# Kernel optimization log

Hardware: AMD Instinct MI355X
Metric: run time of the kernel (lower is better)

Reference implementation:

```python
import jax, jax.numpy as jnp
import numpy as np

N = 100000
E = 1600000
IN_DIM = 128
HID = 64
NUM_CLASSES = 40
K = 3


def setup_inputs() -> dict:
    key = jax.random.key(0)
    ks = jax.random.split(key, 8)
    x = jax.random.normal(ks[0], (N, IN_DIM), dtype=jnp.float32)
    edge_index = jax.random.randint(ks[1], (2, E), 0, N, dtype=jnp.int32)
    s_in = 1.0 / np.sqrt(IN_DIM)
    s_h = 1.0 / np.sqrt(HID)
    W_in = jax.random.uniform(ks[2], (IN_DIM, HID), jnp.float32, -s_in, s_in)
    b_in = jax.random.uniform(ks[3], (HID,), jnp.float32, -s_in, s_in)
    W_layers = jax.random.uniform(ks[4], (K, HID, HID), jnp.float32, -s_h, s_h)
    b_layers = jax.random.uniform(ks[5], (K, HID), jnp.float32, -s_h, s_h)
    W_cls = jax.random.uniform(ks[6], (HID, NUM_CLASSES), jnp.float32, -s_h, s_h)
    b_cls = jax.random.uniform(ks[7], (NUM_CLASSES,), jnp.float32, -s_h, s_h)
    return {"x": x, "edge_index": edge_index, "W_in": W_in, "b_in": b_in,
            "W_layers": W_layers, "b_layers": b_layers, "W_cls": W_cls, "b_cls": b_cls}


def reference(x, edge_index, W_in, b_in, W_layers, b_layers, W_cls, b_cls):
    # eval mode: dropout is identity
    src, dst = edge_index[0], edge_index[1]
    h = jax.nn.relu(x @ W_in + b_in)  # [N, HID]
    for i in range(K):
        # gather messages from src nodes, scatter-add into dst nodes
        agg = jax.ops.segment_sum(h[src], dst, num_segments=N)  # [N, HID]
        h = jax.nn.relu((h + agg) @ W_layers[i] + b_layers[i])
    return h @ W_cls + b_cls  # [N, NUM_CLASSES]
```

## Files before the change

kernel.cpp:

```cpp
#include <hip/hip_runtime.h>
#include <hip/hip_bf16.h>

#define N_NODES 100000
#define E_NUM   1600000
#define IN_DIM  128
#define HID     64
#define NCLS    40
#define NBUCK   782
#define TILE_E  8192
#define NTILE   196
#define BCAP    3072
#define ZROW    N_NODES
#define NTILES_M 6250
#define IN_BLOCKS 1563
#define PREP_BLKS 23

typedef __attribute__((ext_vector_type(8))) short bf16x8;
typedef __attribute__((ext_vector_type(4))) float f32x4;
typedef __attribute__((ext_vector_type(2))) float f32x2;

static __device__ __forceinline__ unsigned short f2bf(float f) {
    unsigned u = __float_as_uint(f);
    u += 0x7FFFu + ((u >> 16) & 1u);
    return (unsigned short)(u >> 16);
}
static __device__ __forceinline__ unsigned pack2bf(float lo, float hi) {
    return (unsigned)f2bf(lo) | ((unsigned)f2bf(hi) << 16);
}

static __device__ __forceinline__ float fp8_1(unsigned b) {
    const unsigned e = (b >> 3) & 15u, m = b & 7u, s = b >> 7;
    float v = e ? __uint_as_float(((e + 120u) << 23) | (m << 20))
                : (float)m * 0.001953125f;
    return s ? -v : v;
}
static __device__ __forceinline__ void dec4(unsigned w, float& x0, float& x1,
                                            float& x2, float& x3) {
#if __has_builtin(__builtin_amdgcn_cvt_pk_f32_fp8)
    f32x2 lo = __builtin_amdgcn_cvt_pk_f32_fp8((int)w, false);
    f32x2 hi = __builtin_amdgcn_cvt_pk_f32_fp8((int)w, true);
    x0 = lo[0]; x1 = lo[1]; x2 = hi[0]; x3 = hi[1];
#else
    x0 = fp8_1(w & 0xFFu);         x1 = fp8_1((w >> 8) & 0xFFu);
    x2 = fp8_1((w >> 16) & 0xFFu); x3 = fp8_1(w >> 24);
#endif
}
static __device__ __forceinline__ unsigned char f2fp8(float f) {
#if __has_builtin(__builtin_amdgcn_cvt_pk_fp8_f32)
    return (unsigned char)(__builtin_amdgcn_cvt_pk_fp8_f32(f, 0.f, 0, false) & 0xFF);
#else
    if (!(f > 0.f)) return 0;
    if (f >= 448.f) return 0x7E;
    unsigned u = __float_as_uint(f);
    u += 0x7FFFFu + ((u >> 20) & 1u);
    const int e = (int)(u >> 23) - 120;
    if (e <= 0) {
        int q = (int)(f * 512.f + 0.5f);
        return (unsigned char)(q > 7 ? 8 : q);
    }
    unsigned r = ((unsigned)e << 3) | ((u >> 20) & 7u);
    return (unsigned char)(r > 0x7Eu ? 0x7Eu : r);
#endif
}

__global__ __launch_bounds__(512) void k_part_prep(
    const int* __restrict__ ei, int* __restrict__ cursor, int* __restrict__ pairs,
    const float* __restrict__ Win, const float* __restrict__ Wl,
    const float* __restrict__ Wc, unsigned* __restrict__ pWin,
    unsigned* __restrict__ pWl, unsigned* __restrict__ pWc,
    unsigned char* __restrict__ H0, unsigned char* __restrict__ H1)
{
    __shared__ int lh[NBUCK];
    __shared__ int lbase[NBUCK];
    __shared__ int lcnt[NBUCK];
    const int t = threadIdx.x;

    if (blockIdx.x < NTILE) {
        for (int i = t; i < NBUCK; i += 512) { lh[i] = 0; lcnt[i] = 0; }
        __syncthreads();
        const int e0 = blockIdx.x * TILE_E;
        #pragma unroll
        for (int k = 0; k < TILE_E; k += 4096) {
            int d[8];
            #pragma unroll
            for (int j = 0; j < 8; ++j) {
                const int e = e0 + k + j * 512 + t;
                d[j] = (e < E_NUM) ? ei[E_NUM + e] : -1;
            }
            #pragma unroll
            for (int j = 0; j < 8; ++j)
                if (d[j] >= 0) atomicAdd(&lh[d[j] >> 7], 1);
        }
        __syncthreads();
        for (int i = t; i < NBUCK; i += 512)
            lbase[i] = lh[i] ? atomicAdd(&cursor[i], lh[i]) : 0;
        __syncthreads();
        #pragma unroll
        for (int k = 0; k < TILE_E; k += 2048) {
            int s[4], d[4];
            #pragma unroll
            for (int j = 0; j < 4; ++j) {
                const int e = e0 + k + j * 512 + t;
                if (e < E_NUM) { s[j] = ei[e]; d[j] = ei[E_NUM + e]; }
                else           { s[j] = -1;    d[j] = -1; }
            }
            #pragma unroll
            for (int j = 0; j < 4; ++j) {
                if (d[j] >= 0) {
                    const int bkt = d[j] >> 7;
                    const int r   = lbase[bkt] + atomicAdd(&lcnt[bkt], 1);
                    if (r < BCAP) pairs[bkt * BCAP + r] = (s[j] << 7) | (d[j] & 127);
                }
            }
        }
        return;
    }

    const int bi = blockIdx.x - NTILE;
    if (bi == 0 && t < 32) {
        if (t < 16) ((unsigned*)(H0 + (size_t)ZROW * HID))[t] = 0;
        else        ((unsigned*)(H1 + (size_t)ZROW * HID))[t - 16] = 0;
    }
    int i = bi * 512 + t;
    if (i < 4096) {
        const int nt = i >> 10, ks = (i >> 8) & 3, ln = (i >> 2) & 63, jp = i & 3;
        const int n = nt * 16 + (ln & 15);
        const int k = ks * 32 + (ln >> 4) * 8 + jp * 2;
        pWin[i] = pack2bf(Win[k * HID + n], Win[(k + 1) * HID + n]);
    } else if (i < 10240) {
        int j = i - 4096;
        const int l = j >> 11; j &= 2047;
        const int nt = j >> 9, ks = (j >> 8) & 1, ln = (j >> 2) & 63, jp = j & 3;
        const int n = nt * 16 + (ln & 15);
        const int k = ks * 32 + (ln >> 4) * 8 + jp * 2;
        const float* w = Wl + (size_t)l * HID * HID;
        pWl[i - 4096] = pack2bf(w[k * HID + n], w[(k + 1) * HID + n]);
    } else if (i < 11776) {
        const int j = i - 10240;
        const int nt = j >> 9, ks = (j >> 8) & 1, ln = (j >> 2) & 63, jp = j & 3;
        const int n = nt * 16 + (ln & 15);
        const int k = ks * 32 + (ln >> 4) * 8 + jp * 2;
        pWc[j] = (n < NCLS) ? pack2bf(Wc[k * NCLS + n], Wc[(k + 1) * NCLS + n]) : 0u;
    }
}

__global__ __launch_bounds__(256) void k_bsort_ingemm(
    const int* __restrict__ cursor, const int* __restrict__ pairs,
    int* __restrict__ srcs, int* __restrict__ row_start, int* __restrict__ row_end,
    const float* __restrict__ x, const unsigned* __restrict__ pWin,
    const float* __restrict__ b, unsigned char* __restrict__ H0)
{
    __shared__ int cnt[128];
    __shared__ int sc[128];
    __shared__ int cur[128];
    const int t = threadIdx.x;

    if (blockIdx.x < NBUCK) {
        const int bk = blockIdx.x;
        const int beg = bk * BCAP;
        const int n_e = min(cursor[bk], BCAP);
        if (t < 128) cnt[t] = 0;
        __syncthreads();
        for (int i = t; i < n_e; i += 1024) {
            const int p0 = pairs[beg + i];
            const int p1 = (i + 256 < n_e) ? pairs[beg + i + 256] : -1;
            const int p2 = (i + 512 < n_e) ? pairs[beg + i + 512] : -1;
            const int p3 = (i + 768 < n_e) ? pairs[beg + i + 768] : -1;
            atomicAdd(&cnt[p0 & 127], 1);
            if (p1 >= 0) atomicAdd(&cnt[p1 & 127], 1);
            if (p2 >= 0) atomicAdd(&cnt[p2 & 127], 1);
            if (p3 >= 0) atomicAdd(&cnt[p3 & 127], 1);
        }
        __syncthreads();
        if (t < 128) sc[t] = (cnt[t] + 7) & ~7;
        __syncthreads();
        for (int off = 1; off < 128; off <<= 1) {
            int a = (t < 128 && t >= off) ? sc[t - off] : 0;
            __syncthreads();
            if (t < 128) sc[t] += a;
            __syncthreads();
        }
        const int node0 = bk << 7;
        if (t < 128) {
            const int pc = (cnt[t] + 7) & ~7;
            const int ex = sc[t] - pc;
            cur[t] = ex;
            const int node = node0 + t;
            if (node < N_NODES) {
                const int rs = beg + ex;
                row_start[node] = rs;
                row_end  [node] = min(rs + pc, beg + BCAP);
            }
            const int fb = beg + ex + cnt[t];
            const int fe = min(beg + ex + pc, beg + BCAP);
            for (int i = fb; i < fe; ++i) srcs[i] = ZROW;
        }
        __syncthreads();
        for (int i = t; i < n_e; i += 1024) {
            const int p0 = pairs[beg + i];
            const int p1 = (i + 256 < n_e) ? pairs[beg + i + 256] : -1;
            const int p2 = (i + 512 < n_e) ? pairs[beg + i + 512] : -1;
            const int p3 = (i + 768 < n_e) ? pairs[beg + i + 768] : -1;
            { const int r = atomicAdd(&cur[p0 & 127], 1); if (r < BCAP) srcs[beg + r] = p0 >> 7; }
            if (p1 >= 0) { const int r = atomicAdd(&cur[p1 & 127], 1); if (r < BCAP) srcs[beg + r] = p1 >> 7; }
            if (p2 >= 0) { const int r = atomicAdd(&cur[p2 & 127], 1); if (r < BCAP) srcs[beg + r] = p2 >> 7; }
            if (p3 >= 0) { const int r = atomicAdd(&cur[p3 & 127], 1); if (r < BCAP) srcs[beg + r] = p3 >> 7; }
        }
        return;
    }

    const int blk  = blockIdx.x - NBUCK;
    const int lane = t & 63;
    const int w    = t >> 6;
    const int tile = blk * 4 + w;
    if (tile >= NTILES_M) return;
    const int quad = lane >> 4;
    const int mrow = lane & 15;
    const int gr   = tile * 16 + mrow;
    const float* xr = x + (size_t)gr * IN_DIM;
    const bf16x8* pb = (const bf16x8*)pWin;

    f32x4 acc0 = {0.f, 0.f, 0.f, 0.f};
    f32x4 acc1 = {0.f, 0.f, 0.f, 0.f};
    f32x4 acc2 = {0.f, 0.f, 0.f, 0.f};
    f32x4 acc3 = {0.f, 0.f, 0.f, 0.f};
    #pragma unroll
    for (int ks = 0; ks < 4; ++ks) {
        const float4 v0 = *(const float4*)(xr + ks * 32 + quad * 8);
        const float4 v1 = *(const float4*)(xr + ks * 32 + quad * 8 + 4);
        union { unsigned u[4]; bf16x8 v; } au;
        au.u[0] = pack2bf(v0.x, v0.y);
        au.u[1] = pack2bf(v0.z, v0.w);
        au.u[2] = pack2bf(v1.x, v1.y);
        au.u[3] = pack2bf(v1.z, v1.w);
        acc0 = __builtin_amdgcn_mfma_f32_16x16x32_bf16(au.v, pb[       ks * 64 + lane], acc0, 0, 0, 0);
        acc1 = __builtin_amdgcn_mfma_f32_16x16x32_bf16(au.v, pb[256 +  ks * 64 + lane], acc1, 0, 0, 0);
        acc2 = __builtin_amdgcn_mfma_f32_16x16x32_bf16(au.v, pb[512 +  ks * 64 + lane], acc2, 0, 0, 0);
        acc3 = __builtin_amdgcn_mfma_f32_16x16x32_bf16(au.v, pb[768 +  ks * 64 + lane], acc3, 0, 0, 0);
    }

    const int colg = lane & 15;
    const int nodeb = tile * 16 + quad * 4;
    const float bv0 = b[     colg];
    const float bv1 = b[16 + colg];
    const float bv2 = b[32 + colg];
    const float bv3 = b[48 + colg];
    #pragma unroll
    for (int r = 0; r < 4; ++r) {
        const size_t ob = (size_t)(nodeb + r) * HID;
        H0[ob      + colg] = f2fp8(fmaxf(acc0[r] + bv0, 0.f));
        H0[ob + 16 + colg] = f2fp8(fmaxf(acc1[r] + bv1, 0.f));
        H0[ob + 32 + colg] = f2fp8(fmaxf(acc2[r] + bv2, 0.f));
        H0[ob + 48 + colg] = f2fp8(fmaxf(acc3[r] + bv3, 0.f));
    }
}

#define ACC8(u) do { \
        dec4((u).x, t0, t1, t2, t3); a0 += t0; a1 += t1; a2 += t2; a3 += t3; \
        dec4((u).y, t0, t1, t2, t3); a4 += t0; a5 += t1; a6 += t2; a7 += t3; } while (0)

#define LOADH(s) (*(const uint2*)(Hin + (size_t)(s) * HID + 8 * fl))

static __device__ __forceinline__ void gather_tile(
    const int* __restrict__ row_start, const int* __restrict__ row_end,
    const int* __restrict__ srcs, const unsigned char* __restrict__ Hin,
    unsigned (*sup)[36], int row0, int t)
{
    const int lane = t & 63;
    const int w    = t >> 6;
    const int nd   = lane >> 4;
    const int sub  = (lane >> 3) & 1;
    const int fl   = lane & 7;
    const int node = row0 + (w << 2) + nd;

    const int rs = row_start[node];
    int rem = row_end[node] - rs;
    if (rem < 0) rem = 0;
    int i = rs + sub;
    const int imax = NBUCK * BCAP - 16;

    const uint2 us = LOADH(node);

    int s0, s1, s2, s3, s4, s5, s6, s7;
    {
        const int ip = min(i, imax);
        s0 = srcs[ip     ]; s1 = srcs[ip +  2];
        s2 = srcs[ip +  4]; s3 = srcs[ip +  6];
        s4 = srcs[ip +  8]; s5 = srcs[ip + 10];
        s6 = srcs[ip + 12]; s7 = srcs[ip + 14];
    }

    float a0 = 0.f, a1 = 0.f, a2 = 0.f, a3 = 0.f;
    float a4 = 0.f, a5 = 0.f, a6 = 0.f, a7 = 0.f;
    float t0, t1, t2, t3;

    for (int nfull = rem >> 4; nfull > 0; --nfull) {
        const uint2 u0 = LOADH(s0); const uint2 u1 = LOADH(s1);
        const uint2 u2 = LOADH(s2); const uint2 u3 = LOADH(s3);
        const uint2 u4 = LOADH(s4); const uint2 u5 = LOADH(s5);
        const uint2 u6 = LOADH(s6); const uint2 u7 = LOADH(s7);
        i += 16;
        const int ip = min(i, imax);
        const int n0 = srcs[ip     ], n1 = srcs[ip +  2];
        const int n2 = srcs[ip +  4], n3 = srcs[ip +  6];
        const int n4 = srcs[ip +  8], n5 = srcs[ip + 10];
        const int n6 = srcs[ip + 12], n7 = srcs[ip + 14];
        ACC8(u0); ACC8(u1); ACC8(u2); ACC8(u3);
        ACC8(u4); ACC8(u5); ACC8(u6); ACC8(u7);
        s0 = n0; s1 = n1; s2 = n2; s3 = n3;
        s4 = n4; s5 = n5; s6 = n6; s7 = n7;
    }
    if (rem & 8) {
        const uint2 u0 = LOADH(s0); const uint2 u1 = LOADH(s1);
        const uint2 u2 = LOADH(s2); const uint2 u3 = LOADH(s3);
        ACC8(u0); ACC8(u1); ACC8(u2); ACC8(u3);
    }

    a0 += __shfl_xor(a0, 8, 64); a1 += __shfl_xor(a1, 8, 64);
    a2 += __shfl_xor(a2, 8, 64); a3 += __shfl_xor(a3, 8, 64);
    a4 += __shfl_xor(a4, 8, 64); a5 += __shfl_xor(a5, 8, 64);
    a6 += __shfl_xor(a6, 8, 64); a7 += __shfl_xor(a7, 8, 64);

    ACC8(us);

    const int r = (w << 2) + nd;
    if (sub == 0) {
        sup[r][4 * fl    ] = pack2bf(a0, a1);
        sup[r][4 * fl + 1] = pack2bf(a2, a3);
    } else {
        sup[r][4 * fl + 2] = pack2bf(a4, a5);
        sup[r][4 * fl + 3] = pack2bf(a6, a7);
    }
}

__global__ __launch_bounds__(256) void k_gather_gemm(
    const int* __restrict__ row_start, const int* __restrict__ row_end,
    const int* __restrict__ srcs,
    const unsigned char* __restrict__ Hin, const unsigned* __restrict__ pWl,
    const float* __restrict__ bl, unsigned char* __restrict__ Hout)
{
    __shared__ unsigned sup[16][36];
    const int t = threadIdx.x;
    const int row0 = blockIdx.x * 16;
    gather_tile(row_start, row_end, srcs, Hin, sup, row0, t);
    __syncthreads();

    const int lane = t & 63;
    const int w    = t >> 6;
    const int quad = lane >> 4;
    const int m    = lane & 15;
    const bf16x8* pb = (const bf16x8*)pWl;
    f32x4 acc = {0.f, 0.f, 0.f, 0.f};
    #pragma unroll
    for (int ks = 0; ks < 2; ++ks) {
        const bf16x8 a  = *(const bf16x8*)&sup[m][ks * 16 + quad * 4];
        const bf16x8 bb = pb[((w << 1) + ks) * 64 + lane];
        acc = __builtin_amdgcn_mfma_f32_16x16x32_bf16(a, bb, acc, 0, 0, 0);
    }
    const int jc = w * 16 + m;
    const float bv = bl[jc];
    #pragma unroll
    for (int r = 0; r < 4; ++r) {
        const int node = row0 + quad * 4 + r;
        Hout[(size_t)node * HID + jc] = f2fp8(fmaxf(acc[r] + bv, 0.f));
    }
}

__global__ __launch_bounds__(256) void k_gather_gemm_cls(
    const int* __restrict__ row_start, const int* __restrict__ row_end,
    const int* __restrict__ srcs,
    const unsigned char* __restrict__ Hin, const unsigned* __restrict__ pWl,
    const float* __restrict__ bl, const unsigned* __restrict__ pWc,
    const float* __restrict__ bc, float* __restrict__ out)
{
    __shared__ unsigned sup[16][36];
    __shared__ unsigned short sh2[16][72];
    const int t = threadIdx.x;
    const int row0 = blockIdx.x * 16;
    gather_tile(row_start, row_end, srcs, Hin, sup, row0, t);
    __syncthreads();

    const int lane = t & 63;
    const int w    = t >> 6;
    const int quad = lane >> 4;
    const int m    = lane & 15;
    const bf16x8* pb = (const bf16x8*)pWl;
    f32x4 acc = {0.f, 0.f, 0.f, 0.f};
    #pragma unroll
    for (int ks = 0; ks < 2; ++ks) {
        const bf16x8 a  = *(const bf16x8*)&sup[m][ks * 16 + quad * 4];
        const bf16x8 bb = pb[((w << 1) + ks) * 64 + lane];
        acc = __builtin_amdgcn_mfma_f32_16x16x32_bf16(a, bb, acc, 0, 0, 0);
    }
    const int jc = w * 16 + m;
    const float bv = bl[jc];
    #pragma unroll
    for (int r = 0; r < 4; ++r)
        sh2[quad * 4 + r][jc] = f2bf(fmaxf(acc[r] + bv, 0.f));
    __syncthreads();

    if (w < 3) {
        const bf16x8* pbc = (const bf16x8*)pWc;
        f32x4 c = {0.f, 0.f, 0.f, 0.f};
        #pragma unroll
        for (int ks = 0; ks < 2; ++ks) {
            const bf16x8 a = *(const bf16x8*)&sh2[m][ks * 32 + quad * 8];
            c = __builtin_amdgcn_mfma_f32_16x16x32_bf16(a, pbc[(w * 2 + ks) * 64 + lane], c, 0, 0, 0);
        }
        const int col = w * 16 + m;
        if (col < NCLS) {
            const float bcv = bc[col];
            #pragma unroll
            for (int r = 0; r < 4; ++r)
                out[(size_t)(row0 + quad * 4 + r) * NCLS + col] = c[r] + bcv;
        }
    }
}

extern "C" void kernel_launch(void* const* d_in, const int* in_sizes, int n_in,
                              void* d_out, int out_size, void* d_ws, size_t ws_size,
                              hipStream_t stream)
{
    const float* x        = (const float*)d_in[0];
    const int*   ei       = (const int*)  d_in[1];
    const float* W_in     = (const float*)d_in[2];
    const float* b_in     = (const float*)d_in[3];
    const float* W_layers = (const float*)d_in[4];
    const float* b_layers = (const float*)d_in[5];
    const float* W_cls    = (const float*)d_in[6];
    const float* b_cls    = (const float*)d_in[7];
    float* out = (float*)d_out;

    unsigned char* H0 = (unsigned char*)d_ws;
    unsigned char* H1 = H0 + (size_t)(N_NODES + 1) * HID;
    int* wsp       = (int*)(H1 + (size_t)(N_NODES + 1) * HID);
    int* pairs     = wsp;
    int* srcs      = wsp + NBUCK * BCAP;
    int* row_start = wsp + 2 * NBUCK * BCAP;
    int* row_end   = row_start + 100096;
    int* cursor    = row_end + 100096;
    unsigned* pWin = (unsigned*)(cursor + 1024);
    unsigned* pWl  = pWin + 4096;
    unsigned* pWc  = pWl + 6144;

    hipMemsetAsync(cursor, 0, 1024 * sizeof(int), stream);

    k_part_prep<<<NTILE + PREP_BLKS, 512, 0, stream>>>(
        ei, cursor, pairs, W_in, W_layers, W_cls, pWin, pWl, pWc, H0, H1);

    k_bsort_ingemm<<<NBUCK + IN_BLOCKS, 256, 0, stream>>>(
        cursor, pairs, srcs, row_start, row_end, x, pWin, b_in, H0);

    const int gemm_blocks = N_NODES / 16;
    k_gather_gemm<<<gemm_blocks, 256, 0, stream>>>(
        row_start, row_end, srcs, H0, pWl,          b_layers,        H1);
    k_gather_gemm<<<gemm_blocks, 256, 0, stream>>>(
        row_start, row_end, srcs, H1, pWl + 2048,   b_layers + HID,  H0);
    k_gather_gemm_cls<<<gemm_blocks, 256, 0, stream>>>(
        row_start, row_end, srcs, H0, pWl + 4096,   b_layers + 2*HID,
        pWc, b_cls, out);
}
```

Baseline: 208.2 us.

## Count degrees during partition and gather with one wave per node

Per-node in-degrees are now counted with global atomics while edges are partitioned, so the bucket-sort kernel no longer needs its first pass over the pairs to build histograms. The gather kernels switch from four nodes per wave to one node per 64-lane wave, using 1024-thread blocks. Each group of 8 lanes handles one edge slot and the partial sums are combined with xor shuffles. This adds 1.6M global atomics to the partition kernel and leaves three quarters of the threads idle during the small MFMA stage, in exchange for more memory-level parallelism per node.

```diff
diff --git a/kernel.cpp b/kernel.cpp
--- a/kernel.cpp
+++ b/kernel.cpp
@@ -65,6 +65,7 @@
 
 __global__ __launch_bounds__(512) void k_part_prep(
     const int* __restrict__ ei, int* __restrict__ cursor, int* __restrict__ pairs,
+    int* __restrict__ deg,
     const float* __restrict__ Win, const float* __restrict__ Wl,
     const float* __restrict__ Wc, unsigned* __restrict__ pWin,
     unsigned* __restrict__ pWl, unsigned* __restrict__ pWc,
@@ -110,6 +111,7 @@
                     const int bkt = d[j] >> 7;
                     const int r   = lbase[bkt] + atomicAdd(&lcnt[bkt], 1);
                     if (r < BCAP) pairs[bkt * BCAP + r] = (s[j] << 7) | (d[j] & 127);
+                    atomicAdd(&deg[d[j]], 1);
                 }
             }
         }
@@ -146,6 +148,7 @@
 
 __global__ __launch_bounds__(256) void k_bsort_ingemm(
     const int* __restrict__ cursor, const int* __restrict__ pairs,
+    const int* __restrict__ deg,
     int* __restrict__ srcs, int* __restrict__ row_start, int* __restrict__ row_end,
     const float* __restrict__ x, const unsigned* __restrict__ pWin,
     const float* __restrict__ b, unsigned char* __restrict__ H0)
@@ -159,20 +162,12 @@
         const int bk = blockIdx.x;
         const int beg = bk * BCAP;
         const int n_e = min(cursor[bk], BCAP);
-        if (t < 128) cnt[t] = 0;
-        __syncthreads();
-        for (int i = t; i < n_e; i += 1024) {
-            const int p0 = pairs[beg + i];
-            const int p1 = (i + 256 < n_e) ? pairs[beg + i + 256] : -1;
-            const int p2 = (i + 512 < n_e) ? pairs[beg + i + 512] : -1;
-            const int p3 = (i + 768 < n_e) ? pairs[beg + i + 768] : -1;
-            atomicAdd(&cnt[p0 & 127], 1);
-            if (p1 >= 0) atomicAdd(&cnt[p1 & 127], 1);
-            if (p2 >= 0) atomicAdd(&cnt[p2 & 127], 1);
-            if (p3 >= 0) atomicAdd(&cnt[p3 & 127], 1);
-        }
-        __syncthreads();
-        if (t < 128) sc[t] = (cnt[t] + 7) & ~7;
+        const int node0 = bk << 7;
+        if (t < 128) {
+            const int c = deg[node0 + t];
+            cnt[t] = c;
+            sc[t] = (c + 7) & ~7;
+        }
         __syncthreads();
         for (int off = 1; off < 128; off <<= 1) {
             int a = (t < 128 && t >= off) ? sc[t - off] : 0;
@@ -180,7 +175,6 @@
             if (t < 128) sc[t] += a;
             __syncthreads();
         }
-        const int node0 = bk << 7;
         if (t < 128) {
             const int pc = (cnt[t] + 7) & ~7;
             const int ex = sc[t] - pc;
@@ -261,79 +255,66 @@
 
 #define LOADH(s) (*(const uint2*)(Hin + (size_t)(s) * HID + 8 * fl))
 
-static __device__ __forceinline__ void gather_tile(
+static __device__ __forceinline__ void gather_tile16(
     const int* __restrict__ row_start, const int* __restrict__ row_end,
     const int* __restrict__ srcs, const unsigned char* __restrict__ Hin,
     unsigned (*sup)[36], int row0, int t)
 {
-    const int lane = t & 63;
-    const int w    = t >> 6;
-    const int nd   = lane >> 4;
-    const int sub  = (lane >> 3) & 1;
-    const int fl   = lane & 7;
-    const int node = row0 + (w << 2) + nd;
+    const int lane  = t & 63;
+    const int wv    = t >> 6;
+    const int eslot = lane >> 3;
+    const int fl    = lane & 7;
+    const int node  = row0 + wv;
 
     const int rs = row_start[node];
     int rem = row_end[node] - rs;
     if (rem < 0) rem = 0;
-    int i = rs + sub;
-    const int imax = NBUCK * BCAP - 16;
+    int i = rs;
 
     const uint2 us = LOADH(node);
-
-    int s0, s1, s2, s3, s4, s5, s6, s7;
-    {
-        const int ip = min(i, imax);
-        s0 = srcs[ip     ]; s1 = srcs[ip +  2];
-        s2 = srcs[ip +  4]; s3 = srcs[ip +  6];
-        s4 = srcs[ip +  8]; s5 = srcs[ip + 10];
-        s6 = srcs[ip + 12]; s7 = srcs[ip + 14];
-    }
 
     float a0 = 0.f, a1 = 0.f, a2 = 0.f, a3 = 0.f;
     float a4 = 0.f, a5 = 0.f, a6 = 0.f, a7 = 0.f;
     float t0, t1, t2, t3;
 
-    for (int nfull = rem >> 4; nfull > 0; --nfull) {
-        const uint2 u0 = LOADH(s0); const uint2 u1 = LOADH(s1);
-        const uint2 u2 = LOADH(s2); const uint2 u3 = LOADH(s3);
-        const uint2 u4 = LOADH(s4); const uint2 u5 = LOADH(s5);
-        const uint2 u6 = LOADH(s6); const uint2 u7 = LOADH(s7);
-        i += 16;
-        const int ip = min(i, imax);
-        const int n0 = srcs[ip     ], n1 = srcs[ip +  2];
-        const int n2 = srcs[ip +  4], n3 = srcs[ip +  6];
-        const int n4 = srcs[ip +  8], n5 = srcs[ip + 10];
-        const int n6 = srcs[ip + 12], n7 = srcs[ip + 14];
-        ACC8(u0); ACC8(u1); ACC8(u2); ACC8(u3);
-        ACC8(u4); ACC8(u5); ACC8(u6); ACC8(u7);
-        s0 = n0; s1 = n1; s2 = n2; s3 = n3;
-        s4 = n4; s5 = n5; s6 = n6; s7 = n7;
-    }
-    if (rem & 8) {
-        const uint2 u0 = LOADH(s0); const uint2 u1 = LOADH(s1);
-        const uint2 u2 = LOADH(s2); const uint2 u3 = LOADH(s3);
-        ACC8(u0); ACC8(u1); ACC8(u2); ACC8(u3);
-    }
-
-    a0 += __shfl_xor(a0, 8, 64); a1 += __shfl_xor(a1, 8, 64);
-    a2 += __shfl_xor(a2, 8, 64); a3 += __shfl_xor(a3, 8, 64);
-    a4 += __shfl_xor(a4, 8, 64); a5 += __shfl_xor(a5, 8, 64);
-    a6 += __shfl_xor(a6, 8, 64); a7 += __shfl_xor(a7, 8, 64);
+    while (rem >= 16) {
+        const int s0 = srcs[i + eslot];
+        const int s1 = srcs[i + 8 + eslot];
+        const uint2 u0 = LOADH(s0);
+        const uint2 u1 = LOADH(s1);
+        ACC8(u0); ACC8(u1);
+        i += 16; rem -= 16;
+    }
+    if (rem) {
+        const int s0 = srcs[i + eslot];
+        const uint2 u0 = LOADH(s0);
+        ACC8(u0);
+    }
+
+    a0 += __shfl_xor(a0,  8, 64); a1 += __shfl_xor(a1,  8, 64);
+    a2 += __shfl_xor(a2,  8, 64); a3 += __shfl_xor(a3,  8, 64);
+    a4 += __shfl_xor(a4,  8, 64); a5 += __shfl_xor(a5,  8, 64);
+    a6 += __shfl_xor(a6,  8, 64); a7 += __shfl_xor(a7,  8, 64);
+    a0 += __shfl_xor(a0, 16, 64); a1 += __shfl_xor(a1, 16, 64);
+    a2 += __shfl_xor(a2, 16, 64); a3 += __shfl_xor(a3, 16, 64);
+    a4 += __shfl_xor(a4, 16, 64); a5 += __shfl_xor(a5, 16, 64);
+    a6 += __shfl_xor(a6, 16, 64); a7 += __shfl_xor(a7, 16, 64);
+    a0 += __shfl_xor(a0, 32, 64); a1 += __shfl_xor(a1, 32, 64);
+    a2 += __shfl_xor(a2, 32, 64); a3 += __shfl_xor(a3, 32, 64);
+    a4 += __shfl_xor(a4, 32, 64); a5 += __shfl_xor(a5, 32, 64);
+    a6 += __shfl_xor(a6, 32, 64); a7 += __shfl_xor(a7, 32, 64);
 
     ACC8(us);
 
-    const int r = (w << 2) + nd;
-    if (sub == 0) {
-        sup[r][4 * fl    ] = pack2bf(a0, a1);
-        sup[r][4 * fl + 1] = pack2bf(a2, a3);
-    } else {
-        sup[r][4 * fl + 2] = pack2bf(a4, a5);
-        sup[r][4 * fl + 3] = pack2bf(a6, a7);
-    }
-}
-
-__global__ __launch_bounds__(256) void k_gather_gemm(
+    if (lane < 8) {
+        sup[wv][4 * fl    ] = pack2bf(a0, a1);
+        sup[wv][4 * fl + 1] = pack2bf(a2, a3);
+        sup[wv][4 * fl + 2] = pack2bf(a4, a5);
+        sup[wv][4 * fl + 3] = pack2bf(a6, a7);
+    }
+}
+
+__global__ __launch_bounds__(1024) void k_gather_gemm(
     const int* __restrict__ row_start, const int* __restrict__ row_end,
     const int* __restrict__ srcs,
     const unsigned char* __restrict__ Hin, const unsigned* __restrict__ pWl,
@@ -342,31 +323,33 @@
     __shared__ unsigned sup[16][36];
     const int t = threadIdx.x;
     const int row0 = blockIdx.x * 16;
-    gather_tile(row_start, row_end, srcs, Hin, sup, row0, t);
+    gather_tile16(row_start, row_end, srcs, Hin, sup, row0, t);
     __syncthreads();
 
-    const int lane = t & 63;
-    const int w    = t >> 6;
-    const int quad = lane >> 4;
-    const int m    = lane & 15;
-    const bf16x8* pb = (const bf16x8*)pWl;
-    f32x4 acc = {0.f, 0.f, 0.f, 0.f};
-    #pragma unroll
-    for (int ks = 0; ks < 2; ++ks) {
-        const bf16x8 a  = *(const bf16x8*)&sup[m][ks * 16 + quad * 4];
-        const bf16x8 bb = pb[((w << 1) + ks) * 64 + lane];
-        acc = __builtin_amdgcn_mfma_f32_16x16x32_bf16(a, bb, acc, 0, 0, 0);
-    }
-    const int jc = w * 16 + m;
-    const float bv = bl[jc];
-    #pragma unroll
-    for (int r = 0; r < 4; ++r) {
-        const int node = row0 + quad * 4 + r;
-        Hout[(size_t)node * HID + jc] = f2fp8(fmaxf(acc[r] + bv, 0.f));
-    }
-}
-
-__global__ __launch_bounds__(256) void k_gather_gemm_cls(
+    if (t < 256) {
+        const int lane = t & 63;
+        const int w    = t >> 6;
+        const int quad = lane >> 4;
+        const int m    = lane & 15;
+        const bf16x8* pb = (const bf16x8*)pWl;
+        f32x4 acc = {0.f, 0.f, 0.f, 0.f};
+        #pragma unroll
+        for (int ks = 0; ks < 2; ++ks) {
+            const bf16x8 a  = *(const bf16x8*)&sup[m][ks * 16 + quad * 4];
+            const bf16x8 bb = pb[((w << 1) + ks) * 64 + lane];
+            acc = __builtin_amdgcn_mfma_f32_16x16x32_bf16(a, bb, acc, 0, 0, 0);
+        }
+        const int jc = w * 16 + m;
+        const float bv = bl[jc];
+        #pragma unroll
+        for (int r = 0; r < 4; ++r) {
+            const int node = row0 + quad * 4 + r;
+            Hout[(size_t)node * HID + jc] = f2fp8(fmaxf(acc[r] + bv, 0.f));
+        }
+    }
+}
+
+__global__ __launch_bounds__(1024) void k_gather_gemm_cls(
     const int* __restrict__ row_start, const int* __restrict__ row_end,
     const int* __restrict__ srcs,
     const unsigned char* __restrict__ Hin, const unsigned* __restrict__ pWl,
@@ -377,26 +360,28 @@
     __shared__ unsigned short sh2[16][72];
     const int t = threadIdx.x;
     const int row0 = blockIdx.x * 16;
-    gather_tile(row_start, row_end, srcs, Hin, sup, row0, t);
+    gather_tile16(row_start, row_end, srcs, Hin, sup, row0, t);
     __syncthreads();
 
     const int lane = t & 63;
     const int w    = t >> 6;
     const int quad = lane >> 4;
     const int m    = lane & 15;
-    const bf16x8* pb = (const bf16x8*)pWl;
-    f32x4 acc = {0.f, 0.f, 0.f, 0.f};
-    #pragma unroll
-    for (int ks = 0; ks < 2; ++ks) {
-        const bf16x8 a  = *(const bf16x8*)&sup[m][ks * 16 + quad * 4];
-        const bf16x8 bb = pb[((w << 1) + ks) * 64 + lane];
-        acc = __builtin_amdgcn_mfma_f32_16x16x32_bf16(a, bb, acc, 0, 0, 0);
-    }
-    const int jc = w * 16 + m;
-    const float bv = bl[jc];
-    #pragma unroll
-    for (int r = 0; r < 4; ++r)
-        sh2[quad * 4 + r][jc] = f2bf(fmaxf(acc[r] + bv, 0.f));
+    if (t < 256) {
+        const bf16x8* pb = (const bf16x8*)pWl;
+        f32x4 acc = {0.f, 0.f, 0.f, 0.f};
+        #pragma unroll
+        for (int ks = 0; ks < 2; ++ks) {
+            const bf16x8 a  = *(const bf16x8*)&sup[m][ks * 16 + quad * 4];
+            const bf16x8 bb = pb[((w << 1) + ks) * 64 + lane];
+            acc = __builtin_amdgcn_mfma_f32_16x16x32_bf16(a, bb, acc, 0, 0, 0);
+        }
+        const int jc = w * 16 + m;
+        const float bv = bl[jc];
+        #pragma unroll
+        for (int r = 0; r < 4; ++r)
+            sh2[quad * 4 + r][jc] = f2bf(fmaxf(acc[r] + bv, 0.f));
+    }
     __syncthreads();
 
     if (w < 3) {
@@ -439,24 +424,25 @@
     int* row_start = wsp + 2 * NBUCK * BCAP;
     int* row_end   = row_start + 100096;
     int* cursor    = row_end + 100096;
-    unsigned* pWin = (unsigned*)(cursor + 1024);
+    int* deg       = cursor + 1024;
+    unsigned* pWin = (unsigned*)(deg + 100096);
     unsigned* pWl  = pWin + 4096;
     unsigned* pWc  = pWl + 6144;
 
-    hipMemsetAsync(cursor, 0, 1024 * sizeof(int), stream);
+    hipMemsetAsync(cursor, 0, (1024 + 100096) * sizeof(int), stream);
 
     k_part_prep<<<NTILE + PREP_BLKS, 512, 0, stream>>>(
-        ei, cursor, pairs, W_in, W_layers, W_cls, pWin, pWl, pWc, H0, H1);
+        ei, cursor, pairs, deg, W_in, W_layers, W_cls, pWin, pWl, pWc, H0, H1);
 
     k_bsort_ingemm<<<NBUCK + IN_BLOCKS, 256, 0, stream>>>(
-        cursor, pairs, srcs, row_start, row_end, x, pWin, b_in, H0);
+        cursor, pairs, deg, srcs, row_start, row_end, x, pWin, b_in, H0);
 
     const int gemm_blocks = N_NODES / 16;
-    k_gather_gemm<<<gemm_blocks, 256, 0, stream>>>(
+    k_gather_gemm<<<gemm_blocks, 1024, 0, stream>>>(
         row_start, row_end, srcs, H0, pWl,          b_layers,        H1);
-    k_gather_gemm<<<gemm_blocks, 256, 0, stream>>>(
+    k_gather_gemm<<<gemm_blocks, 1024, 0, stream>>>(
         row_start, row_end, srcs, H1, pWl + 2048,   b_layers + HID,  H0);
-    k_gather_gemm_cls<<<gemm_blocks, 256, 0, stream>>>(
+    k_gather_gemm_cls<<<gemm_blocks, 1024, 0, stream>>>(
         row_start, row_end, srcs, H0, pWl + 4096,   b_layers + 2*HID,
         pWc, b_cls, out);
 }
```

After: 330.1 us. +58.5%, slower.
